# Kernel optimization log

Hardware: AMD Instinct MI355X
Metric: run time of the kernel (lower is better)

Reference implementation:

```python
import jax, jax.numpy as jnp
import numpy as np

B, IMSIZE, D, L, M, H = 8, 128, 64, 1, 16384, 100
N = B * IMSIZE * IMSIZE


def _build_edges(size, length):
    # build_perception: each pixel connects to all pixels within Chebyshev radius `length`
    ii, jj = np.meshgrid(np.arange(size), np.arange(size), indexing='ij')
    src, dst = [], []
    for dx in range(-length, length + 1):
        for dy in range(-length, length + 1):
            ok = (ii + dx >= 0) & (ii + dx < size) & (jj + dy >= 0) & (jj + dy < size)
            src.append((ii * size + jj)[ok])
            dst.append(((ii + dx) * size + (jj + dy))[ok])
    return np.concatenate(src), np.concatenate(dst)


def setup_inputs() -> dict:
    key = jax.random.key(0)
    ks = jax.random.split(key, 12)
    x = jax.random.normal(ks[0], (N, D), jnp.float32)  # RDN pixel features, flattened
    cluster = jax.random.randint(ks[1], (N,), 0, M).astype(jnp.int32)  # affinity-pool assignment
    s, d = _build_edges(IMSIZE, L)
    offs = (np.arange(B) * IMSIZE * IMSIZE)[:, None]
    edge_src = jnp.asarray((s[None] + offs).reshape(-1), jnp.int32)
    edge_dst = jnp.asarray((d[None] + offs).reshape(-1), jnp.int32)
    ii, jj = np.meshgrid(np.arange(IMSIZE), np.arange(IMSIZE), indexing='ij')
    g = np.stack([ii, jj], -1).reshape(-1, 2).astype(np.float32) / IMSIZE
    coords = jnp.asarray(np.tile(g, (B, 1)))  # spatial_coords.repeat(batch, 1)
    init = lambda k, sh: jax.random.normal(k, sh, jnp.float32) * 0.05
    params = dict(
        W1=init(ks[2], (D + 4, H)), b1=jnp.zeros((H,), jnp.float32),
        W2=init(ks[3], (H, H)), b2=jnp.zeros((H,), jnp.float32),
        W3=init(ks[4], (H, D)), b3=jnp.zeros((D,), jnp.float32),
        Wr=init(ks[5], (D, D)), Wn=init(ks[6], (D, D)), bg=jnp.zeros((D,), jnp.float32),
        Q1w=init(ks[7], (D, H)), Q1b=jnp.zeros((H,), jnp.float32),
        Q2w=init(ks[8], (H, H)), Q2b=jnp.zeros((H,), jnp.float32),
        Q3w=init(ks[9], (H, H)), Q3b=jnp.zeros((H,), jnp.float32),
        Q4w=init(ks[10], (H, 18)), Q4b=jnp.zeros((18,), jnp.float32),
    )
    out = dict(x=x, coords=coords, cluster=cluster, edge_src=edge_src, edge_dst=edge_dst)
    out.update(params)
    return out


def _render_qtr(G, feats):
    # RenderQTR, vectorized over the 3 channels: quadratic texture rendering per pixel
    centers, paras = feats[:, :2], feats[:, 2:20].reshape(-1, 3, 6)
    dx = (G[:, 0] - centers[:, 0])[:, None]
    dy = (G[:, 1] - centers[:, 1])[:, None]
    a, ah, aw, ahh, aww, ahw = (paras[:, :, k] for k in range(6))
    return a + ah * dx + aw * dy + ahh * dx * dx + aww * dy * dy + ahw * dx * dy


def reference(x, coords, cluster, edge_src, edge_dst, W1, b1, W2, b2, W3, b3, Wr, Wn, bg, Q1w, Q1b, Q2w, Q2b, Q3w, Q3b, Q4w, Q4b):
    # --- affinity-aggregation pooling (scatter-mean coarsening) ---
    cnt = jnp.maximum(jax.ops.segment_sum(jnp.ones((N, 1), x.dtype), cluster, num_segments=M), 1.0)
    xp = jax.ops.segment_sum(x, cluster, num_segments=M) / cnt
    cent = jax.ops.segment_sum(coords, cluster, num_segments=M) / cnt          # scatter_mean centroids
    mom = jax.ops.segment_sum(coords * coords, cluster, num_segments=M) / cnt  # scatter_mean moments
    # --- node transform FCBlock on [feat, 10*centroid, 10*moment] ---
    h = jnp.concatenate([xp, 10.0 * cent, 10.0 * mom], axis=-1)
    h = jax.nn.relu(h @ W1 + b1)
    h = jax.nn.relu(h @ W2 + b2)
    h = h @ W3 + b3
    # --- GraphConv(aggr='max') on cluster-coarsened edges (index-chase) ---
    cs, cd = cluster[edge_src], cluster[edge_dst]
    agg = jax.ops.segment_max((h @ Wn)[cs], cd, num_segments=M)
    agg = jnp.where(jnp.isfinite(agg), agg, 0.0)  # empty segments -> 0
    feat = h @ Wr + agg + bg
    # --- node_to_qtr_p2 FCBlock -> joint spatial features ---
    q = jax.nn.relu(feat @ Q1w + Q1b)
    q = jax.nn.relu(q @ Q2w + Q2b)
    q = jax.nn.relu(q @ Q3w + Q3b)
    q = q @ Q4w + Q4b
    jsf = jnp.concatenate([q, cent], axis=-1)[cluster]  # un-pool gather back to pixel nodes
    recon = _render_qtr(coords, jsf)                     # [N, 3]
    return recon.reshape(B, IMSIZE * IMSIZE, 3)          # to_dense_batch (equal-size batches)
```

## Files before the change

### kernel.cpp

```cpp
#include <hip/hip_runtime.h>
#include <hip/hip_fp16.h>
#include <cmath>

#define SSZ    128
#define SS     (SSZ*SSZ)
#define NB     8
#define NNODES (NB*SS)
#define DD     64
#define MM     16384
#define HH     100
#define BINCAP 64
#define KP     136
#define WSLOT  (112*KP)

typedef _Float16 f16x8 __attribute__((ext_vector_type(8)));
typedef float    f32x4 __attribute__((ext_vector_type(4)));

__global__ void k_prep(const float* __restrict__ W1, const float* __restrict__ W2,
                       const float* __restrict__ W3, const float* __restrict__ Wn,
                       const float* __restrict__ Wr, const float* __restrict__ Q1w,
                       const float* __restrict__ Q2w, const float* __restrict__ Q3w,
                       const float* __restrict__ Q4w, __half* __restrict__ Wt) {
    int idx = blockIdx.x * 256 + threadIdx.x;
    if (idx >= 9 * WSLOT) return;
    int mat = idx / WSLOT, rem = idx - mat * WSLOT;
    int n = rem / KP, k = rem - n * KP;
    const float* src; int K, N;
    switch (mat) {
        case 0: src = W1;  K = 68;  N = 100; break;
        case 1: src = W2;  K = 100; N = 100; break;
        case 2: src = W3;  K = 100; N = 64;  break;
        case 3: src = Wn;  K = 64;  N = 64;  break;
        case 4: src = Wr;  K = 64;  N = 64;  break;
        case 5: src = Q1w; K = 64;  N = 100; break;
        case 6: src = Q2w; K = 100; N = 100; break;
        case 7: src = Q3w; K = 100; N = 100; break;
        default:src = Q4w; K = 100; N = 18;  break;
    }
    float v = (n < N && k < K) ? src[k * N + n] : 0.0f;
    Wt[idx] = __float2half(v);
}

__global__ void k_scatter(const int* __restrict__ cluster,
                          int* __restrict__ binCnt, int* __restrict__ nodeList) {
    int n = blockIdx.x * 256 + threadIdx.x;
    if (n >= NNODES) return;
    int c = cluster[n];
    int pos = atomicAdd(&binCnt[c], 1);
    if (pos < BINCAP) nodeList[c * BINCAP + pos] = n;
}

__global__ __launch_bounds__(256) void k_reduce(
    const float* __restrict__ x, const float* __restrict__ coords,
    const int* __restrict__ binCnt, const int* __restrict__ nodeList,
    float* __restrict__ inAll, float* __restrict__ jsf) {
    const int wv = threadIdx.x >> 6, d = threadIdx.x & 63;
    const int c = blockIdx.x * 4 + wv;
    int cnt = binCnt[c];
    if (cnt > BINCAP) cnt = BINCAP;
    int nl = nodeList[c * BINCAP + d];
    float sx = 0.0f, sc = 0.0f, sm = 0.0f;
    for (int i0 = 0; i0 < cnt; i0 += 8) {
        float v[8], cv[8];
        #pragma unroll
        for (int u = 0; u < 8; u++) {
            int i = i0 + u;
            int n = __shfl(nl, i & 63);
            if (i < cnt) {
                v[u]  = x[(size_t)n * 64 + d];
                cv[u] = (d < 2) ? coords[n * 2 + d] : 0.0f;
            } else { v[u] = 0.0f; cv[u] = 0.0f; }
        }
        #pragma unroll
        for (int u = 0; u < 8; u++) {
            sx += v[u]; sc += cv[u]; sm += cv[u] * cv[u];
        }
    }
    float fcnt = fmaxf((float)cnt, 1.0f);
    inAll[c * 68 + d] = sx / fcnt;
    if (d < 2) {
        float cent = sc / fcnt;
        inAll[c * 68 + 64 + d] = 10.0f * cent;
        inAll[c * 68 + 66 + d] = 10.0f * sm / fcnt;
        jsf[c * 20 + 18 + d] = cent;
    }
}

template<int KC, int NT>
__device__ __forceinline__ void mfma_stage(
    const _Float16* __restrict__ inBuf, _Float16* __restrict__ outBuf,
    const _Float16* __restrict__ Wt, const float* __restrict__ bias,
    int Nout, bool relu, int w, int lane) {
    const int m = lane & 15, q = lane >> 4;
    f16x8 a[KC];
    #pragma unroll
    for (int kc = 0; kc < KC; kc++)
        a[kc] = *(const f16x8*)&inBuf[m * KP + kc * 32 + q * 8];
    #pragma unroll
    for (int tt = 0; tt < (NT + 3) / 4; tt++) {
        const int t = w + tt * 4;
        if (t >= NT) break;
        f32x4 acc = {0.0f, 0.0f, 0.0f, 0.0f};
        #pragma unroll
        for (int kc = 0; kc < KC; kc++) {
            f16x8 b = *(const f16x8*)&Wt[(16 * t + m) * KP + kc * 32 + q * 8];
            acc = __builtin_amdgcn_mfma_f32_16x16x32_f16(a[kc], b, acc, 0, 0, 0);
        }
        const int n = 16 * t + m;
        const float bb = (n < Nout) ? bias[n] : 0.0f;
        #pragma unroll
        for (int r = 0; r < 4; r++) {
            float c = acc[r] + bb;
            if (relu) c = fmaxf(c, 0.0f);
            if (n < Nout) outBuf[(q * 4 + r) * KP + n] = (_Float16)c;
        }
    }
}

__global__ __launch_bounds__(256) void k_mlp1(
    const float* __restrict__ inAll, const __half* __restrict__ WtAll,
    const float* __restrict__ b1, const float* __restrict__ b2,
    const float* __restrict__ b3, const float* __restrict__ bg,
    __half* __restrict__ hWnOut, float* __restrict__ featP) {
    __shared__ __align__(16) _Float16 sb0[16 * KP];
    __shared__ __align__(16) _Float16 sb1[16 * KP];
    const _Float16* Wt = (const _Float16*)WtAll;
    const int tid = threadIdx.x, lane = tid & 63, w = tid >> 6;
    const int c0 = blockIdx.x * 16;
    const int m = lane & 15, q = lane >> 4;

    for (int i = tid; i < 16 * 68; i += 256) {
        int r = i / 68, k = i - r * 68;
        sb0[r * KP + k] = (_Float16)inAll[(c0 + r) * 68 + k];
    }
    for (int i = tid; i < 16 * 68; i += 256) {
        int r = i / 68, k = 68 + (i - r * 68);
        sb0[r * KP + k] = (_Float16)0.0f;
    }
    for (int i = tid; i < 16 * 36; i += 256) {
        int r = i / 36, k = 100 + (i - r * 36);
        sb1[r * KP + k] = (_Float16)0.0f;
    }
    __syncthreads();

    mfma_stage<3, 7>(sb0, sb1, Wt + 0 * WSLOT, b1, 100, true,  w, lane);
    __syncthreads();
    mfma_stage<4, 7>(sb1, sb0, Wt + 1 * WSLOT, b2, 100, true,  w, lane);
    __syncthreads();
    mfma_stage<4, 4>(sb0, sb1, Wt + 2 * WSLOT, b3, 64,  false, w, lane);
    __syncthreads();

    {
        const _Float16* Wnt = Wt + 3 * WSLOT;
        const _Float16* Wrt = Wt + 4 * WSLOT;
        f16x8 a0 = *(const f16x8*)&sb1[m * KP + q * 8];
        f16x8 a1 = *(const f16x8*)&sb1[m * KP + 32 + q * 8];
        const int t = w;
        f16x8 bn0 = *(const f16x8*)&Wnt[(16 * t + m) * KP + q * 8];
        f16x8 bn1 = *(const f16x8*)&Wnt[(16 * t + m) * KP + 32 + q * 8];
        f16x8 br0 = *(const f16x8*)&Wrt[(16 * t + m) * KP + q * 8];
        f16x8 br1 = *(const f16x8*)&Wrt[(16 * t + m) * KP + 32 + q * 8];
        f32x4 an = {0.0f, 0.0f, 0.0f, 0.0f};
        f32x4 ar = {0.0f, 0.0f, 0.0f, 0.0f};
        an = __builtin_amdgcn_mfma_f32_16x16x32_f16(a0, bn0, an, 0, 0, 0);
        an = __builtin_amdgcn_mfma_f32_16x16x32_f16(a1, bn1, an, 0, 0, 0);
        ar = __builtin_amdgcn_mfma_f32_16x16x32_f16(a0, br0, ar, 0, 0, 0);
        ar = __builtin_amdgcn_mfma_f32_16x16x32_f16(a1, br1, ar, 0, 0, 0);
        const int n = 16 * t + m;
        const float bgv = bg[n];
        #pragma unroll
        for (int r = 0; r < 4; r++) {
            int row = c0 + q * 4 + r;
            hWnOut[row * 64 + n] = __float2half(an[r]);
            featP [row * 64 + n] = ar[r] + bgv;
        }
    }
}

__global__ __launch_bounds__(512) void k_hvmax(
    const int* __restrict__ cluster, const __half* __restrict__ hWn,
    __half* __restrict__ vmax) {
    __shared__ __half hm[10][16][64];
    const int w = threadIdx.x >> 6, lane = threadIdx.x & 63;
    const int blk  = blockIdx.x;
    const int b    = blk >> 7;
    const int rem  = blk & 127;
    const int r0   = (rem >> 3) << 3;
    const int j0   = (rem & 7) << 4;
    const int base = b * SS;

    for (int lr = w; lr < 10; lr += 8) {
        int gi = r0 - 1 + lr;
        if (gi < 0 || gi >= SSZ) {
            #pragma unroll
            for (int k = 0; k < 16; k++)
                hm[lr][k][lane] = __float2half(-__builtin_inff());
        } else {
            int rowbase = base + gi * SSZ;
            int jl = j0 - 1 + lane;
            int cid = 0;
            if (lane < 18 && jl >= 0 && jl < SSZ) cid = cluster[rowbase + jl];
            float val[18];
            #pragma unroll
            for (int p = 0; p < 18; p++) {
                int jp = j0 - 1 + p;
                int cp = __shfl(cid, p);
                val[p] = (jp >= 0 && jp < SSZ)
                       ? __half2float(hWn[(cp << 6) + lane])
                       : -__builtin_inff();
            }
            #pragma unroll
            for (int k = 0; k < 16; k++)
                hm[lr][k][lane] =
                    __float2half(fmaxf(fmaxf(val[k], val[k + 1]), val[k + 2]));
        }
    }
    __syncthreads();

    const int outbase = (base + (r0 + w) * SSZ + j0) << 6;
    #pragma unroll
    for (int k = 0; k < 16; k++) {
        float v = fmaxf(fmaxf(__half2float(hm[w][k][lane]),
                              __half2float(hm[w + 1][k][lane])),
                        __half2float(hm[w + 2][k][lane]));
        vmax[outbase + (k << 6) + lane] = __float2half(v);
    }
}

__global__ __launch_bounds__(256) void k_cmax(
    const int* __restrict__ binCnt, const int* __restrict__ nodeList,
    const __half* __restrict__ vmax, float* __restrict__ aggF) {
    const int wv = threadIdx.x >> 6, d = threadIdx.x & 63;
    const int c = blockIdx.x * 4 + wv;
    int cnt = binCnt[c];
    if (cnt > BINCAP) cnt = BINCAP;
    int nl = nodeList[c * BINCAP + d];
    float m = -__builtin_inff();
    for (int i0 = 0; i0 < cnt; i0 += 8) {
        float v[8];
        #pragma unroll
        for (int u = 0; u < 8; u++) {
            int i = i0 + u;
            int n = __shfl(nl, i & 63);
            v[u] = (i < cnt) ? __half2float(vmax[((size_t)n << 6) + d])
                             : -__builtin_inff();
        }
        #pragma unroll
        for (int u = 0; u < 8; u++) m = fmaxf(m, v[u]);
    }
    aggF[c * 64 + d] = (cnt == 0) ? 0.0f : m;
}

__global__ __launch_bounds__(256) void k_qmlp(
    const float* __restrict__ featP, const float* __restrict__ aggF,
    const __half* __restrict__ WtAll,
    const float* __restrict__ Q1b, const float* __restrict__ Q2b,
    const float* __restrict__ Q3b, const float* __restrict__ Q4b,
    float* __restrict__ jsf) {
    __shared__ __align__(16) _Float16 sb0[16 * KP];
    __shared__ __align__(16) _Float16 sb1[16 * KP];
    const _Float16* Wt = (const _Float16*)WtAll;
    const int tid = threadIdx.x, lane = tid & 63, w = tid >> 6;
    const int c0 = blockIdx.x * 16;
    const int m = lane & 15, q = lane >> 4;

    for (int i = tid; i < 16 * 64; i += 256) {
        int r = i >> 6, k = i & 63;
        int g = (c0 + r) * 64 + k;
        sb0[r * KP + k] = (_Float16)(featP[g] + aggF[g]);
    }
    for (int i = tid; i < 16 * 36; i += 256) {
        int r = i / 36, k = 100 + (i - r * 36);
        sb0[r * KP + k] = (_Float16)0.0f;
    }
    for (int i = tid; i < 16 * 36; i += 256) {
        int r = i / 36, k = 100 + (i - r * 36);
        sb1[r * KP + k] = (_Float16)0.0f;
    }
    __syncthreads();

    mfma_stage<2, 7>(sb0, sb1, Wt + 5 * WSLOT, Q1b, 100, true, w, lane);
    __syncthreads();
    mfma_stage<4, 7>(sb1, sb0, Wt + 6 * WSLOT, Q2b, 100, true, w, lane);
    __syncthreads();
    mfma_stage<4, 7>(sb0, sb1, Wt + 7 * WSLOT, Q3b, 100, true, w, lane);
    __syncthreads();

    if (w < 2) {
        const _Float16* Q4t = Wt + 8 * WSLOT;
        f16x8 a[4];
        #pragma unroll
        for (int kc = 0; kc < 4; kc++)
            a[kc] = *(const f16x8*)&sb1[m * KP + kc * 32 + q * 8];
        const int t = w;
        f32x4 acc = {0.0f, 0.0f, 0.0f, 0.0f};
        #pragma unroll
        for (int kc = 0; kc < 4; kc++) {
            f16x8 b = *(const f16x8*)&Q4t[(16 * t + m) * KP + kc * 32 + q * 8];
            acc = __builtin_amdgcn_mfma_f32_16x16x32_f16(a[kc], b, acc, 0, 0, 0);
        }
        const int n = 16 * t + m;
        if (n < 18) {
            const float bb = Q4b[n];
            #pragma unroll
            for (int r = 0; r < 4; r++)
                jsf[(c0 + q * 4 + r) * 20 + n] = acc[r] + bb;
        }
    }
}

__global__ void k_render(const float* __restrict__ jsf, const int* __restrict__ cluster,
                         const float* __restrict__ coords, float* __restrict__ out) {
    int n = blockIdx.x * 256 + threadIdx.x;
    if (n >= NNODES) return;
    int c = cluster[n];
    const float* f = &jsf[c * 20];
    float gx = coords[n * 2 + 0], gy = coords[n * 2 + 1];
    float dx = gx - f[0];
    float dy = gy - f[1];
    #pragma unroll
    for (int r = 0; r < 3; r++) {
        float a   = f[2 + r * 6 + 0];
        float ah  = f[2 + r * 6 + 1];
        float aw  = f[2 + r * 6 + 2];
        float ahh = f[2 + r * 6 + 3];
        float aww = f[2 + r * 6 + 4];
        float ahw = f[2 + r * 6 + 5];
        out[n * 3 + r] = a + ah * dx + aw * dy + ahh * dx * dx + aww * dy * dy + ahw * dx * dy;
    }
}

extern "C" void kernel_launch(void* const* d_in, const int* in_sizes, int n_in,
                              void* d_out, int out_size, void* d_ws, size_t ws_size,
                              hipStream_t stream) {
    const float* x       = (const float*)d_in[0];
    const float* coords  = (const float*)d_in[1];
    const int*   cluster = (const int*)  d_in[2];
    const float* W1  = (const float*)d_in[5];
    const float* b1  = (const float*)d_in[6];
    const float* W2  = (const float*)d_in[7];
    const float* b2  = (const float*)d_in[8];
    const float* W3  = (const float*)d_in[9];
    const float* b3  = (const float*)d_in[10];
    const float* Wr  = (const float*)d_in[11];
    const float* Wn  = (const float*)d_in[12];
    const float* bg  = (const float*)d_in[13];
    const float* Q1w = (const float*)d_in[14];
    const float* Q1b = (const float*)d_in[15];
    const float* Q2w = (const float*)d_in[16];
    const float* Q2b = (const float*)d_in[17];
    const float* Q3w = (const float*)d_in[18];
    const float* Q3b = (const float*)d_in[19];
    const float* Q4w = (const float*)d_in[20];
    const float* Q4b = (const float*)d_in[21];
    float* out = (float*)d_out;

    int*    binCnt   = (int*)d_ws;
    int*    nodeList = binCnt + MM;
    float*  inAll    = (float*)(nodeList + MM * BINCAP);
    float*  featP    = inAll + MM * 68;
    float*  aggF     = featP + MM * 64;
    float*  jsf      = aggF  + MM * 64;
    __half* hWnH     = (__half*)(jsf + MM * 20);
    __half* vmaxH    = hWnH + MM * 64;
    __half* WtH      = vmaxH + (size_t)NNODES * 64;

    hipMemsetAsync(binCnt, 0, MM * sizeof(int), stream);
    k_prep   <<<(9 * WSLOT + 255) / 256, 256, 0, stream>>>(W1, W2, W3, Wn, Wr,
                                                           Q1w, Q2w, Q3w, Q4w, WtH);
    k_scatter<<<(NNODES + 255) / 256, 256, 0, stream>>>(cluster, binCnt, nodeList);
    k_reduce <<<MM / 4, 256, 0, stream>>>(x, coords, binCnt, nodeList, inAll, jsf);
    k_mlp1   <<<MM / 16, 256, 0, stream>>>(inAll, WtH, b1, b2, b3, bg, hWnH, featP);
    k_hvmax  <<<1024, 512, 0, stream>>>(cluster, hWnH, vmaxH);
    k_cmax   <<<MM / 4, 256, 0, stream>>>(binCnt, nodeList, vmaxH, aggF);
    k_qmlp   <<<MM / 16, 256, 0, stream>>>(featP, aggF, WtH, Q1b, Q2b, Q3b, Q4b, jsf);
    k_render <<<(NNODES + 255) / 256, 256, 0, stream>>>(jsf, cluster, coords, out);
}
```

Before: 180.2 us.

## Fuse cluster reductions into MLP kernels and pack half2 max in hvmax

The per-cluster mean reduction is folded into the front of k_mlp1, and the per-cluster max of vmax is folded into k_qmlp. This removes two kernel launches and the inAll/aggF round trips through global memory. The binCnt memset moves into k_prep, k_hvmax now works on packed half2 values using half the lanes, and k_render loads the 20-float feature row with float4 loads. The cost is that fewer blocks (one per 16 clusters instead of one per 4) now perform the gather reductions, which lowers the parallelism available for that latency-bound work. The hvmax change also swaps -inf padding for -65504.

```diff
diff --git a/kernel.cpp b/kernel.cpp
--- a/kernel.cpp
+++ b/kernel.cpp
@@ -14,14 +14,24 @@
 #define WSLOT  (112*KP)
 
 typedef _Float16 f16x8 __attribute__((ext_vector_type(8)));
+typedef _Float16 f16x2 __attribute__((ext_vector_type(2)));
 typedef float    f32x4 __attribute__((ext_vector_type(4)));
+
+__device__ __forceinline__ f16x2 hmax2(f16x2 a, f16x2 b) {
+    f16x2 r;
+    r.x = (a.x > b.x) ? a.x : b.x;
+    r.y = (a.y > b.y) ? a.y : b.y;
+    return r;
+}
 
 __global__ void k_prep(const float* __restrict__ W1, const float* __restrict__ W2,
                        const float* __restrict__ W3, const float* __restrict__ Wn,
                        const float* __restrict__ Wr, const float* __restrict__ Q1w,
                        const float* __restrict__ Q2w, const float* __restrict__ Q3w,
-                       const float* __restrict__ Q4w, __half* __restrict__ Wt) {
+                       const float* __restrict__ Q4w, __half* __restrict__ Wt,
+                       int* __restrict__ binCnt) {
     int idx = blockIdx.x * 256 + threadIdx.x;
+    if (idx < MM) binCnt[idx] = 0;
     if (idx >= 9 * WSLOT) return;
     int mat = idx / WSLOT, rem = idx - mat * WSLOT;
     int n = rem / KP, k = rem - n * KP;
@@ -50,42 +60,6 @@
     if (pos < BINCAP) nodeList[c * BINCAP + pos] = n;
 }
 
-__global__ __launch_bounds__(256) void k_reduce(
-    const float* __restrict__ x, const float* __restrict__ coords,
-    const int* __restrict__ binCnt, const int* __restrict__ nodeList,
-    float* __restrict__ inAll, float* __restrict__ jsf) {
-    const int wv = threadIdx.x >> 6, d = threadIdx.x & 63;
-    const int c = blockIdx.x * 4 + wv;
-    int cnt = binCnt[c];
-    if (cnt > BINCAP) cnt = BINCAP;
-    int nl = nodeList[c * BINCAP + d];
-    float sx = 0.0f, sc = 0.0f, sm = 0.0f;
-    for (int i0 = 0; i0 < cnt; i0 += 8) {
-        float v[8], cv[8];
-        #pragma unroll
-        for (int u = 0; u < 8; u++) {
-            int i = i0 + u;
-            int n = __shfl(nl, i & 63);
-            if (i < cnt) {
-                v[u]  = x[(size_t)n * 64 + d];
-                cv[u] = (d < 2) ? coords[n * 2 + d] : 0.0f;
-            } else { v[u] = 0.0f; cv[u] = 0.0f; }
-        }
-        #pragma unroll
-        for (int u = 0; u < 8; u++) {
-            sx += v[u]; sc += cv[u]; sm += cv[u] * cv[u];
-        }
-    }
-    float fcnt = fmaxf((float)cnt, 1.0f);
-    inAll[c * 68 + d] = sx / fcnt;
-    if (d < 2) {
-        float cent = sc / fcnt;
-        inAll[c * 68 + 64 + d] = 10.0f * cent;
-        inAll[c * 68 + 66 + d] = 10.0f * sm / fcnt;
-        jsf[c * 20 + 18 + d] = cent;
-    }
-}
-
 template<int KC, int NT>
 __device__ __forceinline__ void mfma_stage(
     const _Float16* __restrict__ inBuf, _Float16* __restrict__ outBuf,
@@ -118,10 +92,13 @@
 }
 
 __global__ __launch_bounds__(256) void k_mlp1(
-    const float* __restrict__ inAll, const __half* __restrict__ WtAll,
+    const float* __restrict__ x, const float* __restrict__ coords,
+    const int* __restrict__ binCnt, const int* __restrict__ nodeList,
+    const __half* __restrict__ WtAll,
     const float* __restrict__ b1, const float* __restrict__ b2,
     const float* __restrict__ b3, const float* __restrict__ bg,
-    __half* __restrict__ hWnOut, float* __restrict__ featP) {
+    __half* __restrict__ hWnOut, float* __restrict__ featP,
+    float* __restrict__ jsf) {
     __shared__ __align__(16) _Float16 sb0[16 * KP];
     __shared__ __align__(16) _Float16 sb1[16 * KP];
     const _Float16* Wt = (const _Float16*)WtAll;
@@ -129,9 +106,38 @@
     const int c0 = blockIdx.x * 16;
     const int m = lane & 15, q = lane >> 4;
 
-    for (int i = tid; i < 16 * 68; i += 256) {
-        int r = i / 68, k = i - r * 68;
-        sb0[r * KP + k] = (_Float16)inAll[(c0 + r) * 68 + k];
+    #pragma unroll
+    for (int cc = 0; cc < 4; cc++) {
+        const int ci = w * 4 + cc;
+        const int c  = c0 + ci;
+        int cnt = binCnt[c];
+        if (cnt > BINCAP) cnt = BINCAP;
+        int nl = nodeList[c * BINCAP + lane];
+        float sx = 0.0f, sc = 0.0f, sm = 0.0f;
+        for (int i0 = 0; i0 < cnt; i0 += 8) {
+            float v[8], cv[8];
+            #pragma unroll
+            for (int u = 0; u < 8; u++) {
+                int i = i0 + u;
+                int n = __shfl(nl, i & 63);
+                if (i < cnt) {
+                    v[u]  = x[(size_t)n * 64 + lane];
+                    cv[u] = (lane < 2) ? coords[n * 2 + lane] : 0.0f;
+                } else { v[u] = 0.0f; cv[u] = 0.0f; }
+            }
+            #pragma unroll
+            for (int u = 0; u < 8; u++) {
+                sx += v[u]; sc += cv[u]; sm += cv[u] * cv[u];
+            }
+        }
+        float fcnt = fmaxf((float)cnt, 1.0f);
+        sb0[ci * KP + lane] = (_Float16)(sx / fcnt);
+        if (lane < 2) {
+            float cent = sc / fcnt;
+            sb0[ci * KP + 64 + lane] = (_Float16)(10.0f * cent);
+            sb0[ci * KP + 66 + lane] = (_Float16)(10.0f * sm / fcnt);
+            jsf[c * 20 + 18 + lane] = cent;
+        }
     }
     for (int i = tid; i < 16 * 68; i += 256) {
         int r = i / 68, k = 68 + (i - r * 68);
@@ -180,7 +186,7 @@
 __global__ __launch_bounds__(512) void k_hvmax(
     const int* __restrict__ cluster, const __half* __restrict__ hWn,
     __half* __restrict__ vmax) {
-    __shared__ __half hm[10][16][64];
+    __shared__ f16x2 hm[10][16][32];
     const int w = threadIdx.x >> 6, lane = threadIdx.x & 63;
     const int blk  = blockIdx.x;
     const int b    = blk >> 7;
@@ -188,71 +194,52 @@
     const int r0   = (rem >> 3) << 3;
     const int j0   = (rem & 7) << 4;
     const int base = b * SS;
+    const f16x2 NEGH = {(_Float16)-65504.0f, (_Float16)-65504.0f};
 
     for (int lr = w; lr < 10; lr += 8) {
         int gi = r0 - 1 + lr;
         if (gi < 0 || gi >= SSZ) {
-            #pragma unroll
-            for (int k = 0; k < 16; k++)
-                hm[lr][k][lane] = __float2half(-__builtin_inff());
+            if (lane < 32) {
+                #pragma unroll
+                for (int k = 0; k < 16; k++) hm[lr][k][lane] = NEGH;
+            }
         } else {
             int rowbase = base + gi * SSZ;
             int jl = j0 - 1 + lane;
             int cid = 0;
             if (lane < 18 && jl >= 0 && jl < SSZ) cid = cluster[rowbase + jl];
-            float val[18];
+            f16x2 val[18];
             #pragma unroll
             for (int p = 0; p < 18; p++) {
                 int jp = j0 - 1 + p;
                 int cp = __shfl(cid, p);
-                val[p] = (jp >= 0 && jp < SSZ)
-                       ? __half2float(hWn[(cp << 6) + lane])
-                       : -__builtin_inff();
-            }
-            #pragma unroll
-            for (int k = 0; k < 16; k++)
-                hm[lr][k][lane] =
-                    __float2half(fmaxf(fmaxf(val[k], val[k + 1]), val[k + 2]));
+                val[p] = NEGH;
+                if (lane < 32 && jp >= 0 && jp < SSZ)
+                    val[p] = *(const f16x2*)&hWn[(cp << 6) + (lane << 1)];
+            }
+            if (lane < 32) {
+                #pragma unroll
+                for (int k = 0; k < 16; k++)
+                    hm[lr][k][lane] = hmax2(hmax2(val[k], val[k + 1]), val[k + 2]);
+            }
         }
     }
     __syncthreads();
 
     const int outbase = (base + (r0 + w) * SSZ + j0) << 6;
-    #pragma unroll
-    for (int k = 0; k < 16; k++) {
-        float v = fmaxf(fmaxf(__half2float(hm[w][k][lane]),
-                              __half2float(hm[w + 1][k][lane])),
-                        __half2float(hm[w + 2][k][lane]));
-        vmax[outbase + (k << 6) + lane] = __float2half(v);
-    }
-}
-
-__global__ __launch_bounds__(256) void k_cmax(
+    if (lane < 32) {
+        #pragma unroll
+        for (int k = 0; k < 16; k++) {
+            f16x2 v = hmax2(hmax2(hm[w][k][lane], hm[w + 1][k][lane]),
+                            hm[w + 2][k][lane]);
+            *(f16x2*)&vmax[outbase + (k << 6) + (lane << 1)] = v;
+        }
+    }
+}
+
+__global__ __launch_bounds__(256) void k_qmlp(
+    const float* __restrict__ featP, const __half* __restrict__ vmax,
     const int* __restrict__ binCnt, const int* __restrict__ nodeList,
-    const __half* __restrict__ vmax, float* __restrict__ aggF) {
-    const int wv = threadIdx.x >> 6, d = threadIdx.x & 63;
-    const int c = blockIdx.x * 4 + wv;
-    int cnt = binCnt[c];
-    if (cnt > BINCAP) cnt = BINCAP;
-    int nl = nodeList[c * BINCAP + d];
-    float m = -__builtin_inff();
-    for (int i0 = 0; i0 < cnt; i0 += 8) {
-        float v[8];
-        #pragma unroll
-        for (int u = 0; u < 8; u++) {
-            int i = i0 + u;
-            int n = __shfl(nl, i & 63);
-            v[u] = (i < cnt) ? __half2float(vmax[((size_t)n << 6) + d])
-                             : -__builtin_inff();
-        }
-        #pragma unroll
-        for (int u = 0; u < 8; u++) m = fmaxf(m, v[u]);
-    }
-    aggF[c * 64 + d] = (cnt == 0) ? 0.0f : m;
-}
-
-__global__ __launch_bounds__(256) void k_qmlp(
-    const float* __restrict__ featP, const float* __restrict__ aggF,
     const __half* __restrict__ WtAll,
     const float* __restrict__ Q1b, const float* __restrict__ Q2b,
     const float* __restrict__ Q3b, const float* __restrict__ Q4b,
@@ -264,10 +251,28 @@
     const int c0 = blockIdx.x * 16;
     const int m = lane & 15, q = lane >> 4;
 
-    for (int i = tid; i < 16 * 64; i += 256) {
-        int r = i >> 6, k = i & 63;
-        int g = (c0 + r) * 64 + k;
-        sb0[r * KP + k] = (_Float16)(featP[g] + aggF[g]);
+    #pragma unroll
+    for (int cc = 0; cc < 4; cc++) {
+        const int ci = w * 4 + cc;
+        const int c  = c0 + ci;
+        int cnt = binCnt[c];
+        if (cnt > BINCAP) cnt = BINCAP;
+        int nl = nodeList[c * BINCAP + lane];
+        float mx = -__builtin_inff();
+        for (int i0 = 0; i0 < cnt; i0 += 8) {
+            float v[8];
+            #pragma unroll
+            for (int u = 0; u < 8; u++) {
+                int i = i0 + u;
+                int n = __shfl(nl, i & 63);
+                v[u] = (i < cnt) ? __half2float(vmax[((size_t)n << 6) + lane])
+                                 : -__builtin_inff();
+            }
+            #pragma unroll
+            for (int u = 0; u < 8; u++) mx = fmaxf(mx, v[u]);
+        }
+        float agg = (cnt == 0) ? 0.0f : mx;
+        sb0[ci * KP + lane] = (_Float16)(featP[(size_t)c * 64 + lane] + agg);
     }
     for (int i = tid; i < 16 * 36; i += 256) {
         int r = i / 36, k = 100 + (i - r * 36);
@@ -314,18 +319,24 @@
     int n = blockIdx.x * 256 + threadIdx.x;
     if (n >= NNODES) return;
     int c = cluster[n];
-    const float* f = &jsf[c * 20];
+    const float4* f4 = (const float4*)&jsf[c * 20];
+    float fv[20];
+    *(float4*)&fv[0]  = f4[0];
+    *(float4*)&fv[4]  = f4[1];
+    *(float4*)&fv[8]  = f4[2];
+    *(float4*)&fv[12] = f4[3];
+    *(float4*)&fv[16] = f4[4];
     float gx = coords[n * 2 + 0], gy = coords[n * 2 + 1];
-    float dx = gx - f[0];
-    float dy = gy - f[1];
+    float dx = gx - fv[0];
+    float dy = gy - fv[1];
     #pragma unroll
     for (int r = 0; r < 3; r++) {
-        float a   = f[2 + r * 6 + 0];
-        float ah  = f[2 + r * 6 + 1];
-        float aw  = f[2 + r * 6 + 2];
-        float ahh = f[2 + r * 6 + 3];
-        float aww = f[2 + r * 6 + 4];
-        float ahw = f[2 + r * 6 + 5];
+        float a   = fv[2 + r * 6 + 0];
+        float ah  = fv[2 + r * 6 + 1];
+        float aw  = fv[2 + r * 6 + 2];
+        float ahh = fv[2 + r * 6 + 3];
+        float aww = fv[2 + r * 6 + 4];
+        float ahw = fv[2 + r * 6 + 5];
         out[n * 3 + r] = a + ah * dx + aw * dy + ahh * dx * dx + aww * dy * dy + ahw * dx * dy;
     }
 }
@@ -357,22 +368,20 @@
 
     int*    binCnt   = (int*)d_ws;
     int*    nodeList = binCnt + MM;
-    float*  inAll    = (float*)(nodeList + MM * BINCAP);
-    float*  featP    = inAll + MM * 68;
-    float*  aggF     = featP + MM * 64;
-    float*  jsf      = aggF  + MM * 64;
+    float*  featP    = (float*)(nodeList + MM * BINCAP);
+    float*  jsf      = featP + MM * 64;
     __half* hWnH     = (__half*)(jsf + MM * 20);
     __half* vmaxH    = hWnH + MM * 64;
     __half* WtH      = vmaxH + (size_t)NNODES * 64;
 
-    hipMemsetAsync(binCnt, 0, MM * sizeof(int), stream);
     k_prep   <<<(9 * WSLOT + 255) / 256, 256, 0, stream>>>(W1, W2, W3, Wn, Wr,
-                                                           Q1w, Q2w, Q3w, Q4w, WtH);
+                                                           Q1w, Q2w, Q3w, Q4w,
+                                                           WtH, binCnt);
     k_scatter<<<(NNODES + 255) / 256, 256, 0, stream>>>(cluster, binCnt, nodeList);
-    k_reduce <<<MM / 4, 256, 0, stream>>>(x, coords, binCnt, nodeList, inAll, jsf);
-    k_mlp1   <<<MM / 16, 256, 0, stream>>>(inAll, WtH, b1, b2, b3, bg, hWnH, featP);
+    k_mlp1   <<<MM / 16, 256, 0, stream>>>(x, coords, binCnt, nodeList, WtH,
+                                           b1, b2, b3, bg, hWnH, featP, jsf);
     k_hvmax  <<<1024, 512, 0, stream>>>(cluster, hWnH, vmaxH);
-    k_cmax   <<<MM / 4, 256, 0, stream>>>(binCnt, nodeList, vmaxH, aggF);
-    k_qmlp   <<<MM / 16, 256, 0, stream>>>(featP, aggF, WtH, Q1b, Q2b, Q3b, Q4b, jsf);
+    k_qmlp   <<<MM / 16, 256, 0, stream>>>(featP, vmaxH, binCnt, nodeList, WtH,
+                                           Q1b, Q2b, Q3b, Q4b, jsf);
     k_render <<<(NNODES + 255) / 256, 256, 0, stream>>>(jsf, cluster, coords, out);
 }
```

Result: no change. 181.0 us (+0.5%).
